# Optimization experiments

Hardware: AMD Instinct MI355X
Metric: run time of the kernel (lower is better)

The kernel has to match this reference:

```python
import jax, jax.numpy as jnp
import numpy as np

ROUTINGS = 3


def squash(v):
    # squash along last axis: v/|v| * |v|^2/(1+|v|^2)
    norm = jnp.linalg.norm(v, axis=-1, keepdims=True)
    ns = norm * norm
    return v / norm * (ns / (1.0 + ns))


def setup_inputs() -> dict:
    key = jax.random.key(0)
    k1, k2 = jax.random.split(key)
    B, N, I, D, Din = 256, 10, 1152, 16, 8
    inputs = jax.random.normal(k1, (B, I, Din), dtype=jnp.float32)
    # glorot-uniform-ish init for W [N, I, D, Din]
    limit = np.sqrt(6.0 / (D + Din)).astype(np.float32)
    W = jax.random.uniform(k2, (N, I, D, Din), dtype=jnp.float32,
                           minval=-limit, maxval=limit)
    return {"inputs": inputs, "W": W}


def reference(inputs, W):
    # inputs: [B, I, Din], W: [N, I, D, Din]
    # u_hat[b,n,i,d] = sum_k W[n,i,d,k] * inputs[b,i,k]  (replaces tf.map_fn)
    u_hat = jnp.einsum('nidk,bik->bnid', W, inputs)  # [B, N, I, D]
    b = jnp.zeros(u_hat.shape[:3], dtype=u_hat.dtype)  # [B, N, I]
    outputs = None
    for r in range(ROUTINGS):
        c = jax.nn.softmax(b, axis=1)  # softmax over output capsules N
        outputs = squash(jnp.einsum('bni,bnid->bnd', c, u_hat))  # [B, N, D]
        if r < ROUTINGS - 1:
            # agreement: a[b,n,i] = <outputs[b,n,:], u_hat[b,n,i,:]>
            b = b + jnp.einsum('bnd,bnid->bni', outputs, u_hat)
    return outputs
```

## Files before the change

### kernel.cpp

```cpp
#include <hip/hip_runtime.h>
#include <hip/hip_bf16.h>
#include <stdint.h>


#define BN 256
#define NN 10
#define II 1152
#define DD 16
#define KK 8
#define NT 18
#define NP 5
#define NCH 3
#define CHI 384

typedef unsigned short ushort_t;
typedef unsigned int uint_t;

__device__ __forceinline__ float bflo(uint_t u) {
    union { uint_t i; float f; } v; v.i = u << 16; return v.f;
}
__device__ __forceinline__ float bfhi(uint_t u) {
    union { uint_t i; float f; } v; v.i = u & 0xffff0000u; return v.f;
}
__device__ __forceinline__ uint_t pkbf(float lo, float hi) {
    __hip_bfloat162 h = __float22bfloat162_rn(make_float2(lo, hi));
    uint_t u; __builtin_memcpy(&u, &h, sizeof(u)); return u;
}

__global__ __launch_bounds__(256) void caps_uhat_s0(const float* __restrict__ xg,
                                                    const float* __restrict__ wg,
                                                    ushort_t* __restrict__ u,
                                                    float* __restrict__ part0,
                                                    int b0, int c4)
{
    __shared__ float wlds[4][2048];
    __shared__ float redn[4][64][2];
    const int tid = threadIdx.x;
    const int lane = tid & 63, wv = tid >> 6;
    const int dq = lane & 3, il = lane >> 2;
    const int nb8 = gridDim.x >> 3;
    const int L   = (blockIdx.x & 7) * nb8 + (blockIdx.x >> 3);
    const int it  = L / (NP * c4);
    const int rem = L - it * (NP * c4);
    const int np  = rem / c4;
    const int bl  = (rem - np * c4) * 4;
    const int n0  = np * 2;
    const int i = it * 64 + wv * 16 + il;

    const bool h0 = (il & 1), h1 = (il >> 1) & 1, h2 = (il >> 2) & 1, h3 = (il >> 3) & 1;
    float* myred = &redn[wv][lane][0];
    float* mylds = &wlds[wv][0];
    const int lrow = lane >> 5, lc = lane & 31;
    const float4* wtile0 = (const float4*)(wg + (size_t)(n0 * II + it * 64 + wv * 16) * (DD * KK));

#define STAGE_W(NNV)                                                         \
    {                                                                        \
        const float4* wt = wtile0 + (size_t)(NNV) * II * 32;                 \
        _Pragma("unroll")                                                    \
        for (int j = 0; j < 8; ++j) {                                        \
            int row = lrow + 2 * j;                                          \
            int chunk = row * 32 + (lc ^ (row & 7));                         \
            __builtin_amdgcn_global_load_lds(                                \
                (const __attribute__((address_space(1))) void*)(wt + chunk), \
                (__attribute__((address_space(3))) void*)(mylds + j * 256),  \
                16, 0, 0);                                                   \
        }                                                                    \
    }

    STAGE_W(0);

    float xv[4][8];
#pragma unroll
    for (int bb = 0; bb < 4; ++bb) {
        const float4* xp = (const float4*)(xg + ((size_t)(b0 + bl + bb) * II + i) * KK);
        float4 x0 = xp[0], x1 = xp[1];
        xv[bb][0] = x0.x; xv[bb][1] = x0.y; xv[bb][2] = x0.z; xv[bb][3] = x0.w;
        xv[bb][4] = x1.x; xv[bb][5] = x1.y; xv[bb][6] = x1.z; xv[bb][7] = x1.w;
    }

    auto compute_n = [&](int n, const float4* w, int slot) {
        float s[4][4];
#pragma unroll
        for (int dj = 0; dj < 4; ++dj) {
            float4 wa = w[2 * dj], wb = w[2 * dj + 1];
#pragma unroll
            for (int bb = 0; bb < 4; ++bb) {
                s[bb][dj] = wa.x * xv[bb][0] + wa.y * xv[bb][1]
                          + wa.z * xv[bb][2] + wa.w * xv[bb][3]
                          + wb.x * xv[bb][4] + wb.y * xv[bb][5]
                          + wb.z * xv[bb][6] + wb.w * xv[bb][7];
            }
        }
#pragma unroll
        for (int bb = 0; bb < 4; ++bb) {
            uint2 q;
            q.x = pkbf(s[bb][0], s[bb][1]);
            q.y = pkbf(s[bb][2], s[bb][3]);
            *(uint2*)(u + (((size_t)(bl + bb) * NN + n) * II + i) * DD + dq * 4) = q;
        }
        float v8[8];
#pragma unroll
        for (int k = 0; k < 8; ++k) {
            float a0 = s[(2 * k) >> 2][(2 * k) & 3];
            float a1 = s[(2 * k + 1) >> 2][(2 * k + 1) & 3];
            float give = h0 ? a0 : a1;
            float got  = __shfl_xor(give, 4, 64);
            v8[k] = (h0 ? a1 : a0) + got;
        }
        float v4[4];
#pragma unroll
        for (int k = 0; k < 4; ++k) {
            float a0 = v8[2 * k], a1 = v8[2 * k + 1];
            float give = h1 ? a0 : a1;
            float got  = __shfl_xor(give, 8, 64);
            v4[k] = (h1 ? a1 : a0) + got;
        }
        float v2[2];
#pragma unroll
        for (int k = 0; k < 2; ++k) {
            float a0 = v4[2 * k], a1 = v4[2 * k + 1];
            float give = h2 ? a0 : a1;
            float got  = __shfl_xor(give, 16, 64);
            v2[k] = (h2 ? a1 : a0) + got;
        }
        {
            float a0 = v2[0], a1 = v2[1];
            float give = h3 ? a0 : a1;
            float got  = __shfl_xor(give, 32, 64);
            myred[slot] = (h3 ? a1 : a0) + got;
        }
    };

    float4 w[8];
    asm volatile("s_waitcnt vmcnt(0)" ::: "memory");
#pragma unroll
    for (int jj = 0; jj < 8; ++jj)
        w[jj] = *(const float4*)(mylds + il * 128 + dq * 32 + ((jj ^ (il & 7)) << 2));
    asm volatile("s_waitcnt lgkmcnt(0)" ::: "memory");
    STAGE_W(1);
    compute_n(n0, w, 0);

    asm volatile("s_waitcnt vmcnt(0)" ::: "memory");
#pragma unroll
    for (int jj = 0; jj < 8; ++jj)
        w[jj] = *(const float4*)(mylds + il * 128 + dq * 32 + ((jj ^ (il & 7)) << 2));
    compute_n(n0 + 1, w, 1);
#undef STAGE_W

    __syncthreads();
    if (tid < 128) {
        int bb = tid >> 5, r5 = tid & 31, nn = r5 >> 4, d = r5 & 15;
        int lane2 = ((bb * 4 + (d & 3)) << 2) + (d >> 2);
        float v = redn[0][lane2][nn] + redn[1][lane2][nn]
                + redn[2][lane2][nn] + redn[3][lane2][nn];
        part0[((size_t)(b0 + bl + bb) * NT + it) * 160 + (n0 + nn) * 16 + d] = 0.1f * v;
    }
}

__device__ __forceinline__ void block_reduce_part(float sp[NN][4], int tid,
                                                  float* red,
                                                  float* __restrict__ partp)
{
#pragma unroll
    for (int m = 4; m <= 32; m <<= 1)
#pragma unroll
        for (int n = 0; n < NN; ++n)
#pragma unroll
            for (int j = 0; j < 4; ++j)
                sp[n][j] += __shfl_xor(sp[n][j], m, 64);

    const int lane = tid & 63, wv = tid >> 6, ld = tid & 3;
    if (lane < 4) {
#pragma unroll
        for (int n = 0; n < NN; ++n)
#pragma unroll
            for (int j = 0; j < 4; ++j)
                red[(wv * NN + n) * 16 + ld * 4 + j] = sp[n][j];
    }
    __syncthreads();
    if (tid < 160) {
        int n = tid >> 4, dd = tid & 15;
        float v = 0.f;
#pragma unroll
        for (int w = 0; w < 4; ++w) v += red[(w * NN + n) * 16 + dd];
        partp[tid] = v;
    }
}

__global__ __launch_bounds__(256) void caps_sweep(const ushort_t* __restrict__ u,
                                                  const float* __restrict__ p0,
                                                  const float* __restrict__ p1,
                                                  float* __restrict__ pout, int b0)
{
    __shared__ float red[4 * 160];
    __shared__ float o_s[160];
    const int tid = threadIdx.x, g = tid >> 2, ld = tid & 3;
    const int cb = blockIdx.x / NCH, ch = blockIdx.x % NCH;
    const int b = b0 + cb;
    const ushort_t* ub = u + (size_t)cb * (NN * II * DD);
    const int i0 = ch * CHI + g;

#define ULOAD(R, S)                                                            \
    _Pragma("unroll")                                                          \
    for (int n = 0; n < NN; ++n)                                               \
        R[n] = *(const uint2*)(ub + ((size_t)(n * II + i0 + (S) * 64)) * DD + ld * 4);

    uint2 rA[NN], rB[NN], rC[NN];
    ULOAD(rA, 0)
    ULOAD(rB, 1)

    if (tid < 160) {
        float v = 0.f;
#pragma unroll
        for (int t = 0; t < NT; ++t)
            v += p0[((size_t)b * NT + t) * 160 + tid];
        float sq = v * v;
#pragma unroll
        for (int m = 1; m <= 8; m <<= 1) sq += __shfl_xor(sq, m, 64);
        float o = v * (sqrtf(sq) / (1.0f + sq));
        if (p1) {
            float v1 = 0.f;
#pragma unroll
            for (int c2 = 0; c2 < NCH; ++c2)
                v1 += p1[((size_t)b * NCH + c2) * 160 + tid];
            float sq1 = v1 * v1;
#pragma unroll
            for (int m = 1; m <= 8; m <<= 1) sq1 += __shfl_xor(sq1, m, 64);
            o += v1 * (sqrtf(sq1) / (1.0f + sq1));
        }
        o_s[tid] = o;
    }
    __syncthreads();

    float sp[NN][4];
#pragma unroll
    for (int n = 0; n < NN; ++n)
#pragma unroll
        for (int j = 0; j < 4; ++j) sp[n][j] = 0.f;

#define STEP(R)                                                                \
    {                                                                          \
        float p[NN];                                                           \
        _Pragma("unroll")                                                      \
        for (int n = 0; n < NN; ++n) {                                         \
            float4 o4 = *(const float4*)&o_s[(n << 4) + (ld << 2)];            \
            p[n] = bflo(R[n].x) * o4.x + bfhi(R[n].x) * o4.y                   \
                 + bflo(R[n].y) * o4.z + bfhi(R[n].y) * o4.w;                  \
        }                                                                      \
        float a[NN];                                                           \
        _Pragma("unroll")                                                      \
        for (int n = 0; n < NN; ++n) {                                         \
            float t2 = p[n] + __shfl_xor(p[n], 1, 64);                         \
            a[n] = t2 + __shfl_xor(t2, 2, 64);                                 \
        }                                                                      \
        float m01 = fmaxf(fmaxf(a[0], a[1]), a[2]);                            \
        float m2  = fmaxf(fmaxf(a[3], a[4]), a[5]);                            \
        float m3  = fmaxf(fmaxf(a[6], a[7]), a[8]);                            \
        float mx  = fmaxf(fmaxf(m01, m2), fmaxf(m3, a[9]));                    \
        float c[NN];                                                           \
        _Pragma("unroll")                                                      \
        for (int n = 0; n < NN; ++n) c[n] = __expf(a[n] - mx);                 \
        float s01 = c[0] + c[1], s23 = c[2] + c[3], s45 = c[4] + c[5];         \
        float s67 = c[6] + c[7], s89 = c[8] + c[9];                            \
        float ssum = ((s01 + s23) + (s45 + s67)) + s89;                        \
        float inv = 1.0f / ssum;                                               \
        _Pragma("unroll")                                                      \
        for (int n = 0; n < NN; ++n) {                                         \
            float w = c[n] * inv;                                              \
            sp[n][0] += w * bflo(R[n].x); sp[n][1] += w * bfhi(R[n].x);        \
            sp[n][2] += w * bflo(R[n].y); sp[n][3] += w * bfhi(R[n].y);        \
        }                                                                      \
    }

    ULOAD(rC, 2)  STEP(rA)
    ULOAD(rA, 3)  STEP(rB)
    ULOAD(rB, 4)  STEP(rC)
    ULOAD(rC, 5)  STEP(rA)
    STEP(rB)
    STEP(rC)
#undef ULOAD
#undef STEP

    block_reduce_part(sp, tid, red, pout + ((size_t)b * NCH + ch) * 160);
}

__global__ __launch_bounds__(192) void caps_out(const float* __restrict__ p2,
                                                float* __restrict__ out, int b0)
{
    const int b = b0 + blockIdx.x;
    const int t = threadIdx.x;
    if (t < 160) {
        float v = 0.f;
#pragma unroll
        for (int ch = 0; ch < NCH; ++ch)
            v += p2[((size_t)b * NCH + ch) * 160 + t];
        float sq = v * v;
#pragma unroll
        for (int m = 1; m <= 8; m <<= 1) sq += __shfl_xor(sq, m, 64);
        out[(size_t)b * 160 + t] = v * (sqrtf(sq) / (1.0f + sq));
    }
}

extern "C" void kernel_launch(void* const* d_in, const int* in_sizes, int n_in,
                              void* d_out, int out_size, void* d_ws, size_t ws_size,
                              hipStream_t stream)
{
    const float* xg = (const float*)d_in[0];
    const float* wg = (const float*)d_in[1];
    if (n_in >= 2 && in_sizes[0] == NN * II * DD * KK) {
        const float* t = xg; xg = wg; wg = t;
    }
    float* outp = (float*)d_out;

    const size_t perB  = (size_t)NN * II * DD * 2;
    const size_t p0B   = (size_t)BN * NT * 160 * 4;
    const size_t p12B  = (size_t)BN * NCH * 160 * 4;
    size_t extra = p0B + 2 * p12B;
    size_t avail = (ws_size > extra) ? ws_size - extra : 0;
    int C = 256;
    if (avail < (size_t)256 * perB) {
        C = (int)(avail / perB);
        C &= ~15;
        if (C < 16) C = 16;
    }
    ushort_t* uws = (ushort_t*)d_ws;
    float* part0 = (float*)((char*)d_ws + (size_t)C * perB);
    float* part1 = part0 + (size_t)BN * NT * 160;
    float* part2 = part1 + (size_t)BN * NCH * 160;

    for (int b0 = 0; b0 < BN; b0 += C) {
        int c = (BN - b0 < C) ? (BN - b0) : C;
        int c4 = c / 4;
        caps_uhat_s0<<<NT * NP * c4, 256, 0, stream>>>(xg, wg, uws, part0, b0, c4);
        caps_sweep  <<<c * NCH, 256, 0, stream>>>(uws, part0, nullptr, part1, b0);
        caps_sweep  <<<c * NCH, 256, 0, stream>>>(uws, part0, part1,  part2, b0);
        caps_out    <<<c,       192, 0, stream>>>(part2, outp, b0);
    }
}
```

Before: 136.9 us.

## Fuse both routing sweeps and output squash into one 1024-thread kernel per batch

```diff
diff --git a/kernel.cpp b/kernel.cpp
--- a/kernel.cpp
+++ b/kernel.cpp
@@ -10,8 +10,6 @@
 #define KK 8
 #define NT 18
 #define NP 5
-#define NCH 3
-#define CHI 384
 
 typedef unsigned short ushort_t;
 typedef unsigned int uint_t;
@@ -157,9 +155,8 @@
     }
 }
 
-__device__ __forceinline__ void block_reduce_part(float sp[NN][4], int tid,
-                                                  float* red,
-                                                  float* __restrict__ partp)
+__device__ __forceinline__ void block_reduce16(float sp[NN][4], int tid,
+                                               float* red, float* outv)
 {
 #pragma unroll
     for (int m = 4; m <= 32; m <<= 1)
@@ -168,77 +165,48 @@
 #pragma unroll
             for (int j = 0; j < 4; ++j)
                 sp[n][j] += __shfl_xor(sp[n][j], m, 64);
-
-    const int lane = tid & 63, wv = tid >> 6, ld = tid & 3;
+    const int lane = tid & 63, wv = tid >> 6, ldq = tid & 3;
     if (lane < 4) {
 #pragma unroll
         for (int n = 0; n < NN; ++n)
 #pragma unroll
             for (int j = 0; j < 4; ++j)
-                red[(wv * NN + n) * 16 + ld * 4 + j] = sp[n][j];
+                red[wv * 160 + n * 16 + ldq * 4 + j] = sp[n][j];
     }
     __syncthreads();
     if (tid < 160) {
         int n = tid >> 4, dd = tid & 15;
         float v = 0.f;
 #pragma unroll
-        for (int w = 0; w < 4; ++w) v += red[(w * NN + n) * 16 + dd];
-        partp[tid] = v;
-    }
-}
-
-__global__ __launch_bounds__(256) void caps_sweep(const ushort_t* __restrict__ u,
-                                                  const float* __restrict__ p0,
-                                                  const float* __restrict__ p1,
-                                                  float* __restrict__ pout, int b0)
+        for (int w = 0; w < 16; ++w) v += red[w * 160 + n * 16 + dd];
+        outv[tid] = v;
+    }
+    __syncthreads();
+}
+
+__global__ __launch_bounds__(1024) void caps_route(const ushort_t* __restrict__ u,
+                                                   const float* __restrict__ p0,
+                                                   float* __restrict__ out, int b0)
 {
-    __shared__ float red[4 * 160];
+    __shared__ float red[16 * 160];
     __shared__ float o_s[160];
-    const int tid = threadIdx.x, g = tid >> 2, ld = tid & 3;
-    const int cb = blockIdx.x / NCH, ch = blockIdx.x % NCH;
-    const int b = b0 + cb;
-    const ushort_t* ub = u + (size_t)cb * (NN * II * DD);
-    const int i0 = ch * CHI + g;
+    __shared__ float s_s[160];
+    const int tid = threadIdx.x, g2 = tid >> 2, ld = tid & 3;
+    const int b = b0 + blockIdx.x;
+    const ushort_t* ub = u + (size_t)blockIdx.x * (NN * II * DD);
+    const float tmask = (1024 + g2 < II) ? 1.f : 0.f;
+    const int  tidx  = (1024 + g2 < II) ? (1024 + g2) : (II - 1);
 
 #define ULOAD(R, S)                                                            \
     _Pragma("unroll")                                                          \
     for (int n = 0; n < NN; ++n)                                               \
-        R[n] = *(const uint2*)(ub + ((size_t)(n * II + i0 + (S) * 64)) * DD + ld * 4);
-
-    uint2 rA[NN], rB[NN], rC[NN];
-    ULOAD(rA, 0)
-    ULOAD(rB, 1)
-
-    if (tid < 160) {
-        float v = 0.f;
-#pragma unroll
-        for (int t = 0; t < NT; ++t)
-            v += p0[((size_t)b * NT + t) * 160 + tid];
-        float sq = v * v;
-#pragma unroll
-        for (int m = 1; m <= 8; m <<= 1) sq += __shfl_xor(sq, m, 64);
-        float o = v * (sqrtf(sq) / (1.0f + sq));
-        if (p1) {
-            float v1 = 0.f;
-#pragma unroll
-            for (int c2 = 0; c2 < NCH; ++c2)
-                v1 += p1[((size_t)b * NCH + c2) * 160 + tid];
-            float sq1 = v1 * v1;
-#pragma unroll
-            for (int m = 1; m <= 8; m <<= 1) sq1 += __shfl_xor(sq1, m, 64);
-            o += v1 * (sqrtf(sq1) / (1.0f + sq1));
-        }
-        o_s[tid] = o;
-    }
-    __syncthreads();
-
-    float sp[NN][4];
-#pragma unroll
-    for (int n = 0; n < NN; ++n)
-#pragma unroll
-        for (int j = 0; j < 4; ++j) sp[n][j] = 0.f;
-
-#define STEP(R)                                                                \
+        R[n] = *(const uint2*)(ub + ((size_t)(n * II + (S) * 256 + g2)) * DD + ld * 4);
+#define ULOADT(R)                                                              \
+    _Pragma("unroll")                                                          \
+    for (int n = 0; n < NN; ++n)                                               \
+        R[n] = *(const uint2*)(ub + ((size_t)(n * II + tidx)) * DD + ld * 4);
+
+#define STEP(R, MK)                                                            \
     {                                                                          \
         float p[NN];                                                           \
         _Pragma("unroll")                                                      \
@@ -263,7 +231,7 @@
         float s01 = c[0] + c[1], s23 = c[2] + c[3], s45 = c[4] + c[5];         \
         float s67 = c[6] + c[7], s89 = c[8] + c[9];                            \
         float ssum = ((s01 + s23) + (s45 + s67)) + s89;                        \
-        float inv = 1.0f / ssum;                                               \
+        float inv = (MK) / ssum;                                               \
         _Pragma("unroll")                                                      \
         for (int n = 0; n < NN; ++n) {                                         \
             float w = c[n] * inv;                                              \
@@ -272,33 +240,66 @@
         }                                                                      \
     }
 
-    ULOAD(rC, 2)  STEP(rA)
-    ULOAD(rA, 3)  STEP(rB)
-    ULOAD(rB, 4)  STEP(rC)
-    ULOAD(rC, 5)  STEP(rA)
-    STEP(rB)
-    STEP(rC)
+#define PASS                                                                   \
+    {                                                                          \
+        uint2 rA[NN], rB[NN];                                                  \
+        ULOAD(rA, 0)                                                           \
+        ULOAD(rB, 1)  STEP(rA, 1.f)                                            \
+        ULOAD(rA, 2)  STEP(rB, 1.f)                                            \
+        ULOAD(rB, 3)  STEP(rA, 1.f)                                            \
+        ULOADT(rA)    STEP(rB, 1.f)                                            \
+        STEP(rA, tmask)                                                        \
+    }
+
+    if (tid < 160) {
+        float v = 0.f;
+#pragma unroll
+        for (int t = 0; t < NT; ++t)
+            v += p0[((size_t)b * NT + t) * 160 + tid];
+        float sq = v * v;
+#pragma unroll
+        for (int m = 1; m <= 8; m <<= 1) sq += __shfl_xor(sq, m, 64);
+        o_s[tid] = v * (sqrtf(sq) / (1.0f + sq));
+    }
+    __syncthreads();
+
+    float sp[NN][4];
+#pragma unroll
+    for (int n = 0; n < NN; ++n)
+#pragma unroll
+        for (int j = 0; j < 4; ++j) sp[n][j] = 0.f;
+
+    PASS
+    block_reduce16(sp, tid, red, s_s);
+
+    if (tid < 160) {
+        float v = s_s[tid];
+        float sq = v * v;
+#pragma unroll
+        for (int m = 1; m <= 8; m <<= 1) sq += __shfl_xor(sq, m, 64);
+        o_s[tid] = o_s[tid] + v * (sqrtf(sq) / (1.0f + sq));
+    }
+    __syncthreads();
+
+#pragma unroll
+    for (int n = 0; n < NN; ++n)
+#pragma unroll
+        for (int j = 0; j < 4; ++j) sp[n][j] = 0.f;
+
+    PASS
+    block_reduce16(sp, tid, red, s_s);
+
+    if (tid < 160) {
+        float v = s_s[tid];
+        float sq = v * v;
+#pragma unroll
+        for (int m = 1; m <= 8; m <<= 1) sq += __shfl_xor(sq, m, 64);
+        out[(size_t)b * 160 + tid] = v * (sqrtf(sq) / (1.0f + sq));
+    }
 #undef ULOAD
+#undef ULOADT
 #undef STEP
-
-    block_reduce_part(sp, tid, red, pout + ((size_t)b * NCH + ch) * 160);
-}
-
-__global__ __launch_bounds__(192) void caps_out(const float* __restrict__ p2,
-                                                float* __restrict__ out, int b0)
-{
-    const int b = b0 + blockIdx.x;
-    const int t = threadIdx.x;
-    if (t < 160) {
-        float v = 0.f;
-#pragma unroll
-        for (int ch = 0; ch < NCH; ++ch)
-            v += p2[((size_t)b * NCH + ch) * 160 + t];
-        float sq = v * v;
-#pragma unroll
-        for (int m = 1; m <= 8; m <<= 1) sq += __shfl_xor(sq, m, 64);
-        out[(size_t)b * 160 + t] = v * (sqrtf(sq) / (1.0f + sq));
-    }
+#undef PASS
 }
 
 extern "C" void kernel_launch(void* const* d_in, const int* in_sizes, int n_in,
@@ -314,8 +315,7 @@
 
     const size_t perB  = (size_t)NN * II * DD * 2;
     const size_t p0B   = (size_t)BN * NT * 160 * 4;
-    const size_t p12B  = (size_t)BN * NCH * 160 * 4;
-    size_t extra = p0B + 2 * p12B;
+    size_t extra = p0B;
     size_t avail = (ws_size > extra) ? ws_size - extra : 0;
     int C = 256;
     if (avail < (size_t)256 * perB) {
@@ -325,15 +325,11 @@
     }
     ushort_t* uws = (ushort_t*)d_ws;
     float* part0 = (float*)((char*)d_ws + (size_t)C * perB);
-    float* part1 = part0 + (size_t)BN * NT * 160;
-    float* part2 = part1 + (size_t)BN * NCH * 160;
 
     for (int b0 = 0; b0 < BN; b0 += C) {
         int c = (BN - b0 < C) ? (BN - b0) : C;
         int c4 = c / 4;
         caps_uhat_s0<<<NT * NP * c4, 256, 0, stream>>>(xg, wg, uws, part0, b0, c4);
-        caps_sweep  <<<c * NCH, 256, 0, stream>>>(uws, part0, nullptr, part1, b0);
-        caps_sweep  <<<c * NCH, 256, 0, stream>>>(uws, part0, part1,  part2, b0);
-        caps_out    <<<c,       192, 0, stream>>>(part2, outp, b0);
-    }
-}
+        caps_route  <<<c, 1024, 0, stream>>>(uws, part0, outp, b0);
+    }
+}
```

New measurement: 234.2 us. 71.1% more time.
